# Performance work log

Hardware: AMD Instinct MI355X
Metric: run time of the kernel (lower is better)

## Reference

```python
import jax, jax.numpy as jnp
import numpy as np

EPS = 1e-05

def exp_map_at_origin(v, c):
    sqrt_c = jnp.sqrt(c)
    v_norm = jnp.maximum(jnp.linalg.norm(v, axis=-1, keepdims=True), EPS)
    return (1.0 / sqrt_c) * jnp.tanh(sqrt_c * v_norm) * (v / v_norm)

def log_map_at_origin(y, c):
    sqrt_c = jnp.sqrt(c)
    y_norm = jnp.maximum(jnp.linalg.norm(y, axis=-1, keepdims=True), EPS)
    y_norm_clamped = jnp.minimum(y_norm, 1.0 / sqrt_c - EPS)
    return (1.0 / sqrt_c) * jnp.arctanh(sqrt_c * y_norm_clamped) * (y / y_norm)

def poincare_distance(x, y, c):
    # x, y: [B, H, S, d]; returns [B, H, S, S]
    sqrt_c = jnp.sqrt(c)
    xns = jnp.sum(x * x, axis=-1, keepdims=True)          # [B,H,S,1]
    yns = jnp.sum(y * y, axis=-1, keepdims=True)          # [B,H,S,1]
    xy = jnp.einsum('bhsd,bhtd->bhst', x, y)
    xnsb = xns                                            # broadcast over t
    ynsb = jnp.swapaxes(yns, -2, -1)                      # [B,H,1,S]
    diff_norm_sq = xnsb - 2.0 * xy + ynsb
    denom = jnp.maximum((1.0 - c * xnsb) * (1.0 - c * ynsb), EPS)
    arg = jnp.maximum(1.0 + 2.0 * c * diff_norm_sq / denom, 1.0 + EPS)
    return (1.0 / sqrt_c) * jnp.arccosh(arg)

def setup_inputs() -> dict:
    key = jax.random.key(0)
    ks = jax.random.split(key, 5)
    B, S, D = 2, 1024, 1024
    x = jax.random.normal(ks[0], (B, S, D), dtype=jnp.float32)
    scale = 0.02
    W_q = scale * jax.random.normal(ks[1], (D, D), dtype=jnp.float32)
    W_k = scale * jax.random.normal(ks[2], (D, D), dtype=jnp.float32)
    W_v = scale * jax.random.normal(ks[3], (D, D), dtype=jnp.float32)
    W_o = scale * jax.random.normal(ks[4], (D, D), dtype=jnp.float32)
    return {
        'x': x, 'W_q': W_q, 'W_k': W_k, 'W_v': W_v, 'W_o': W_o,
        'log_c': jnp.zeros((), jnp.float32),
        'beta': jnp.zeros((), jnp.float32),
        'attention_bias': jnp.zeros((), jnp.float32),
    }

def reference(x, W_q, W_k, W_v, W_o, log_c, beta, attention_bias):
    B, S, D = x.shape
    H = 16
    dh = D // H
    c = jax.nn.softplus(log_c)
    beta_pos = jax.nn.softplus(beta)

    def split_heads(t):  # [B,S,D] -> [B,H,S,dh]
        return jnp.transpose(t.reshape(B, S, H, dh), (0, 2, 1, 3))

    q_t = split_heads(x @ W_q.T)
    k_t = split_heads(x @ W_k.T)
    v_t = split_heads(x @ W_v.T)

    q_h = exp_map_at_origin(q_t, c)
    k_h = exp_map_at_origin(k_t, c)
    v_h = exp_map_at_origin(v_t, c)

    dist = poincare_distance(q_h, k_h, c)                 # [B,H,S,S]
    scores = -beta_pos * dist - attention_bias
    weights = jax.nn.softmax(scores, axis=-1)

    v_tan = log_map_at_origin(v_h, c)
    out_tan = jnp.einsum('bhst,bhtd->bhsd', weights, v_tan)
    out_hyp = exp_map_at_origin(out_tan, c)
    out_heads_tan = log_map_at_origin(out_hyp, c)

    concat = jnp.transpose(out_heads_tan, (0, 2, 1, 3)).reshape(B, S, D)
    return concat @ W_o.T
```

## Files before the change

### kernel.cpp

```cpp
#include <hip/hip_runtime.h>
#include <math.h>


#define EPS_ 1e-5f

constexpr int Ss = 1024, Dd = 1024, Hh = 16, DHh = 64;

typedef __attribute__((ext_vector_type(8))) short bf16x8;
typedef __attribute__((ext_vector_type(4))) short s16x4;
typedef __attribute__((ext_vector_type(4))) float f32x4;

__device__ __forceinline__ float softplusf_(float x) {
    return (x > 20.f) ? x : log1pf(expf(x));
}
__device__ __forceinline__ short f2bf(float f) {
    union { float f; unsigned u; } v; v.f = f;
    unsigned r = v.u + 0x7FFFu + ((v.u >> 16) & 1u);
    return (short)(r >> 16);
}
__device__ __forceinline__ unsigned pks(short a, short b) {
    return (unsigned)(unsigned short)a | ((unsigned)(unsigned short)b << 16);
}

#if __has_builtin(__builtin_amdgcn_cvt_pk_bf16_f32)
typedef __attribute__((ext_vector_type(2))) __bf16 bfp2;
__device__ __forceinline__ unsigned cvtpk(float a, float b) {
    union { bfp2 v; unsigned u; } x;
    x.v = __builtin_amdgcn_cvt_pk_bf16_f32(a, b);
    return x.u;
}
#else
__device__ __forceinline__ unsigned cvtpk(float a, float b) { return pks(f2bf(a), f2bf(b)); }
#endif

#if __has_builtin(__builtin_amdgcn_sqrtf)
#define FSQRT __builtin_amdgcn_sqrtf
#else
#define FSQRT sqrtf
#endif
#if __has_builtin(__builtin_amdgcn_logf)
#define FLOG2 __builtin_amdgcn_logf
#else
#define FLOG2 __log2f
#endif
#if __has_builtin(__builtin_amdgcn_exp2f)
#define FEXP2 __builtin_amdgcn_exp2f
#else
#define FEXP2 exp2f
#endif

__device__ __forceinline__ void gload_lds16(const short* gp, short* lp) {
    __builtin_amdgcn_global_load_lds(
        (__attribute__((address_space(1))) void*)(void*)(const_cast<short*>(gp)),
        (__attribute__((address_space(3))) void*)(void*)(lp), 16, 0, 0);
}

__global__ __launch_bounds__(256) void split_all(
    const float* __restrict__ x,  const float* __restrict__ Wq,
    const float* __restrict__ Wk, const float* __restrict__ Wv,
    const float* __restrict__ Wo,
    short* __restrict__ xh,  short* __restrict__ wqh,
    short* __restrict__ wkh, short* __restrict__ wvh, short* __restrict__ woh)
{
    int g = blockIdx.x * 256 + threadIdx.x;
    const float* src; short* dst; int base;
    if (g < 524288)       { src = x;  dst = xh;  base = g; }
    else if (g < 786432)  { src = Wq; dst = wqh; base = g - 524288; }
    else if (g < 1048576) { src = Wk; dst = wkh; base = g - 786432; }
    else if (g < 1310720) { src = Wv; dst = wvh; base = g - 1048576; }
    else                  { src = Wo; dst = woh; base = g - 1310720; }
    float4 v = *(const float4*)(src + (size_t)base * 4);
    uint2 hp; hp.x = cvtpk(v.x, v.y); hp.y = cvtpk(v.z, v.w);
    *(uint2*)(dst + (size_t)base * 4) = hp;
}

__global__ __launch_bounds__(256, 3) void gemm_qkv(
    const short* __restrict__ Ap,
    const short* __restrict__ Wq, const short* __restrict__ Wk, const short* __restrict__ Wv,
    short* __restrict__ qh, short* __restrict__ kh, short* __restrict__ vtT,
    float* __restrict__ qnsT, float2* __restrict__ knpk,
    const float* __restrict__ p_logc)
{
    const int z = blockIdx.z;
    const short* Bp = (z == 0) ? Wq : (z == 1 ? Wk : Wv);
    const int K = 1024;

    __shared__ short As[128 * 64];
    __shared__ short Bs[64 * 64];

    const int tid = threadIdx.x;
    const int wv = tid >> 6, lane = tid & 63, quad = lane >> 4, l15 = lane & 15;
    const int bm = blockIdx.y * 128, bn = blockIdx.x * 64;

    const int lr8 = lane >> 3, lc8 = lane & 7;
    const int swz8 = (lc8 ^ lr8) * 8;

    const short* gAl = Ap + (size_t)(bm + lr8) * K + swz8;
    const short* gBl = Bp + (size_t)(bn + lr8) * K + swz8;

    f32x4 acc[2][4];
#pragma unroll
    for (int mt = 0; mt < 2; mt++)
#pragma unroll
        for (int j = 0; j < 4; j++) acc[mt][j] = (f32x4){0.f, 0.f, 0.f, 0.f};

    for (int k0 = 0; k0 < K; k0 += 64) {
        __syncthreads();
#pragma unroll
        for (int i = 0; i < 4; i++)
            gload_lds16(gAl + (size_t)((wv * 4 + i) * 8) * K + k0, &As[(wv * 4 + i) * 512]);
#pragma unroll
        for (int j = 0; j < 2; j++)
            gload_lds16(gBl + (size_t)((wv * 2 + j) * 8) * K + k0, &Bs[(wv * 2 + j) * 512]);
        __syncthreads();
#pragma unroll
        for (int w = 0; w < 2; w++) {
            const int xs = ((w * 4 + quad) ^ (l15 & 7)) * 8;
            bf16x8 fa0 = *(const bf16x8*)&As[(wv * 32 + l15) * 64 + xs];
            bf16x8 fa1 = *(const bf16x8*)&As[(wv * 32 + 16 + l15) * 64 + xs];
#pragma unroll
            for (int nt = 0; nt < 4; nt++) {
                bf16x8 fb = *(const bf16x8*)&Bs[(nt * 16 + l15) * 64 + xs];
                acc[0][nt] = __builtin_amdgcn_mfma_f32_16x16x32_bf16(fa0, fb, acc[0][nt], 0, 0, 0);
                acc[1][nt] = __builtin_amdgcn_mfma_f32_16x16x32_bf16(fa1, fb, acc[1][nt], 0, 0, 0);
            }
        }
    }

    const float c = softplusf_(p_logc[0]);
    const float sc = sqrtf(c);
    const float twoC = 2.f * c;
    const int h0 = blockIdx.x;

    if (z < 2) {
        short* yout = (z == 0) ? qh : kh;
#pragma unroll
        for (int mt = 0; mt < 2; mt++) {
            const int mbase = bm + wv * 32 + mt * 16;
            float fr[4];
#pragma unroll
            for (int r = 0; r < 4; r++) {
                float s2 = 0.f;
#pragma unroll
                for (int nt = 0; nt < 4; nt++) s2 += acc[mt][nt][r] * acc[mt][nt][r];
#pragma unroll
                for (int mk = 1; mk < 16; mk <<= 1) s2 += __shfl_xor(s2, mk, 64);
                float n = fmaxf(sqrtf(s2), EPS_);
                float fac = tanhf(sc * n) / (sc * n);
                fr[r] = fac;
                if (l15 == 0) {
                    int m = mbase + quad * 4 + r;
                    int bI = m >> 10, s = m & 1023;
                    float yns = s2 * fac * fac;
                    if (z == 0) {
                        qnsT[(size_t)(bI * Hh + h0) * Ss + s] = yns;
                    } else {
                        knpk[(size_t)(bI * Hh + h0) * Ss + s]
                            = make_float2(yns, twoC / (1.f - c * yns));
                    }
                }
            }
#pragma unroll
            for (int nt = 0; nt < 4; nt++)
#pragma unroll
                for (int r = 0; r < 4; r++) {
                    int m = mbase + quad * 4 + r;
                    yout[(size_t)m * Dd + bn + nt * 16 + l15] = f2bf(acc[mt][nt][r] * fr[r]);
                }
        }
    } else {
#pragma unroll
        for (int mt = 0; mt < 2; mt++) {
            const int mbase = bm + wv * 32 + mt * 16;
            float tr[4];
#pragma unroll
            for (int r = 0; r < 4; r++) {
                float s2 = 0.f;
#pragma unroll
                for (int nt = 0; nt < 4; nt++) s2 += acc[mt][nt][r] * acc[mt][nt][r];
#pragma unroll
                for (int mk = 1; mk < 16; mk <<= 1) s2 += __shfl_xor(s2, mk, 64);
                float n = fmaxf(sqrtf(s2), EPS_);
                float fac = tanhf(sc * n) / (sc * n);
                float yn = n * fac;
                float ycl = fminf(yn, 1.f / sc - EPS_);
                float f2 = atanhf(sc * ycl) / (sc * fmaxf(yn, EPS_));
                tr[r] = fac * f2;
            }
            const int m0 = mbase + quad * 4;
            const int bI = m0 >> 10, s0 = m0 & 1023;
            const int w6 = s0 & 63;
            const int s0p = (s0 & ~63)
                          | ((w6 >> 5) * 32 + ((w6 & 15) >> 2) * 8 + ((w6 >> 4) & 1) * 4);
#pragma unroll
            for (int nt = 0; nt < 4; nt++) {
                int d = nt * 16 + l15;
                uint2 pk;
                pk.x = cvtpk(acc[mt][nt][0] * tr[0], acc[mt][nt][1] * tr[1]);
                pk.y = cvtpk(acc[mt][nt][2] * tr[2], acc[mt][nt][3] * tr[3]);
                *(uint2*)&vtT[((size_t)(bI * Hh + h0) * DHh + d) * Ss + s0p] = pk;
            }
        }
    }
}

__global__ __launch_bounds__(512) void attn_mfma(
    const short* __restrict__ qh, const short* __restrict__ kh, const short* __restrict__ vtT,
    const float* __restrict__ qnsT, const float2* __restrict__ knpk,
    short* __restrict__ ccb,
    const float* __restrict__ p_logc, const float* __restrict__ p_beta)
{
    const float c = softplusf_(p_logc[0]);
    const float sc = sqrtf(c);
    const float bp = softplusf_(p_beta[0]);
    const float nkc = -bp / sc;
    const float cap = 2.f * c * 1e5f;
    const float onePlus = 1.f + EPS_;

    const int bh = blockIdx.x, qt = blockIdx.y;
    const int b = bh >> 4, h = bh & 15;
    const int tid = threadIdx.x;
    const int wv = tid >> 6, lane = tid & 63;
    const int g = wv >> 2, w4 = wv & 3;
    const int quad = lane >> 4, l15 = lane & 15;
    const int q = qt * 64 + w4 * 16 + l15;

    __shared__ short Ks[2][2][4096];
    __shared__ short Vt[2][2][4096];

    const short* qb = qh + (size_t)(b * Ss + q) * Dd + h * DHh + quad * 8;
    bf16x8 qf0 = *(const bf16x8*)qb;
    bf16x8 qf1 = *(const bf16x8*)(qb + 32);

    const float qn = qnsT[(size_t)bh * Ss + q];
    const float irq = 1.f / (1.f - c * qn);

    f32x4 O4[4];
#pragma unroll
    for (int nt = 0; nt < 4; nt++) O4[nt] = (f32x4){0.f, 0.f, 0.f, 0.f};
    float lac = 0.f;

    const int tbase = g * 512;
    const int lr8 = lane >> 3, lc8 = lane & 7;
    const float2* nb = knpk + (size_t)bh * Ss;
    const short* ksb = kh + (size_t)b * Ss * Dd + h * DHh + (lc8 ^ lr8) * 8;
    const short* vsb = vtT + (size_t)bh * DHh * Ss + tbase + (lc8 ^ lr8) * 8;

    f32x4 nA0[4], nA1[4], nB0[4], nB1[4];

#pragma unroll
    for (int j = 0; j < 2; j++) {
        const int R = w4 * 16 + j * 8;
        gload_lds16(ksb + (size_t)(tbase + R + lr8) * Dd, &Ks[g][0][R * 64]);
        gload_lds16(vsb + (size_t)(R + lr8) * Ss, &Vt[g][0][R * 64]);
        gload_lds16(ksb + (size_t)(tbase + 64 + R + lr8) * Dd, &Ks[g][1][R * 64]);
        gload_lds16(vsb + (size_t)(R + lr8) * Ss + 64, &Vt[g][1][R * 64]);
    }
#pragma unroll
    for (int nt = 0; nt < 4; nt++) {
        const float2* np = nb + tbase + nt * 16 + quad * 4;
        nA0[nt] = *(const f32x4*)np;
        nA1[nt] = *(const f32x4*)(np + 2);
    }
    __syncthreads();

    const int xsl = (quad ^ (l15 & 7)) * 8;

#pragma unroll
    for (int ch = 0; ch < 8; ch++) {
        const int cur = ch & 1;

        bf16x8 k0[4], k1[4], v0[4], v1[4];
#pragma unroll
        for (int nt = 0; nt < 4; nt++) {
            k0[nt] = *(const bf16x8*)&Ks[g][cur][(nt * 16 + l15) * 64 + xsl];
            k1[nt] = *(const bf16x8*)&Ks[g][cur][(nt * 16 + l15) * 64 + (xsl ^ 32)];
        }
#pragma unroll
        for (int nt = 0; nt < 4; nt++) {
            v0[nt] = *(const bf16x8*)&Vt[g][cur][(nt * 16 + l15) * 64 + xsl];
            v1[nt] = *(const bf16x8*)&Vt[g][cur][(nt * 16 + l15) * 64 + (xsl ^ 32)];
        }

        f32x4 acc[4];
        __builtin_amdgcn_s_setprio(1);
#pragma unroll
        for (int nt = 0; nt < 4; nt++) {
            f32x4 a = (f32x4){0.f, 0.f, 0.f, 0.f};
            a = __builtin_amdgcn_mfma_f32_16x16x32_bf16(k0[nt], qf0, a, 0, 0, 0);
            a = __builtin_amdgcn_mfma_f32_16x16x32_bf16(k1[nt], qf1, a, 0, 0, 0);
            acc[nt] = a;
        }
        __builtin_amdgcn_s_setprio(0);

        if (ch < 7) __syncthreads();

        if (ch + 2 < 8) {
#pragma unroll
            for (int j = 0; j < 2; j++) {
                const int R = w4 * 16 + j * 8;
                gload_lds16(ksb + (size_t)(tbase + (ch + 2) * 64 + R + lr8) * Dd,
                            &Ks[g][cur][R * 64]);
                gload_lds16(vsb + (size_t)(R + lr8) * Ss + (ch + 2) * 64,
                            &Vt[g][cur][R * 64]);
            }
        }
        if (ch + 1 < 8) {
#pragma unroll
            for (int nt = 0; nt < 4; nt++) {
                const float2* np = nb + tbase + (ch + 1) * 64 + nt * 16 + quad * 4;
                if ((ch & 1) == 0) { nB0[nt] = *(const f32x4*)np; nB1[nt] = *(const f32x4*)(np + 2); }
                else               { nA0[nt] = *(const f32x4*)np; nA1[nt] = *(const f32x4*)(np + 2); }
            }
        }

        float sv[4][4];
#pragma unroll
        for (int nt = 0; nt < 4; nt++) {
#pragma unroll
            for (int r = 0; r < 4; r++) {
                float kn, ik2c;
                if ((ch & 1) == 0) {
                    kn   = (r < 2) ? nA0[nt][(r & 1) * 2]     : nA1[nt][(r & 1) * 2];
                    ik2c = (r < 2) ? nA0[nt][(r & 1) * 2 + 1] : nA1[nt][(r & 1) * 2 + 1];
                } else {
                    kn   = (r < 2) ? nB0[nt][(r & 1) * 2]     : nB1[nt][(r & 1) * 2];
                    ik2c = (r < 2) ? nB0[nt][(r & 1) * 2 + 1] : nB1[nt][(r & 1) * 2 + 1];
                }
                float dns = (qn + kn) - 2.f * acc[nt][r];
                float co  = fminf(irq * ik2c, cap);
                float arg = fmaxf(fmaf(co, dns, 1.f), onePlus);
                float u   = arg + FSQRT(fmaf(arg, arg, -1.f));
                float p   = FEXP2(nkc * FLOG2(u));
                sv[nt][r] = p;
                lac += p;
            }
        }

        union { unsigned u[4]; bf16x8 v; } p0, p1;
        p0.u[0] = cvtpk(sv[0][0], sv[0][1]); p0.u[1] = cvtpk(sv[0][2], sv[0][3]);
        p0.u[2] = cvtpk(sv[1][0], sv[1][1]); p0.u[3] = cvtpk(sv[1][2], sv[1][3]);
        p1.u[0] = cvtpk(sv[2][0], sv[2][1]); p1.u[1] = cvtpk(sv[2][2], sv[2][3]);
        p1.u[2] = cvtpk(sv[3][0], sv[3][1]); p1.u[3] = cvtpk(sv[3][2], sv[3][3]);

        __builtin_amdgcn_s_setprio(1);
#pragma unroll
        for (int nt = 0; nt < 4; nt++) {
            O4[nt] = __builtin_amdgcn_mfma_f32_16x16x32_bf16(v0[nt], p0.v, O4[nt], 0, 0, 0);
            O4[nt] = __builtin_amdgcn_mfma_f32_16x16x32_bf16(v1[nt], p1.v, O4[nt], 0, 0, 0);
        }
        __builtin_amdgcn_s_setprio(0);
    }

    lac += __shfl_xor(lac, 16, 64);
    lac += __shfl_xor(lac, 32, 64);

    float* Ored = (float*)&Ks[0][0][0];
    float* lred = (float*)&Vt[0][0][0];
    __syncthreads();
    if (g == 1) {
#pragma unroll
        for (int nt = 0; nt < 4; nt++)
#pragma unroll
            for (int r = 0; r < 4; r++)
                Ored[((w4 * 4 + nt) * 16 + (quad * 4 + r)) * 16 + l15] = O4[nt][r];
        if (lane < 16) lred[w4 * 16 + lane] = lac;
    }
    __syncthreads();

    if (g == 0) {
        const float lt = lac + lred[w4 * 16 + l15];
        const float il = 1.f / lt;
        float ot[4][4], t2 = 0.f;
#pragma unroll
        for (int nt = 0; nt < 4; nt++)
#pragma unroll
            for (int r = 0; r < 4; r++) {
                float v = (O4[nt][r]
                    + Ored[((w4 * 4 + nt) * 16 + (quad * 4 + r)) * 16 + l15]) * il;
                ot[nt][r] = v;
                t2 += v * v;
            }
        t2 += __shfl_xor(t2, 16, 64);
        t2 += __shfl_xor(t2, 32, 64);

        float n = fmaxf(sqrtf(t2), EPS_);
        float fac = tanhf(sc * n) / (sc * n);
        float y2 = t2 * fac * fac;
        float yn = fmaxf(sqrtf(y2), EPS_);
        float ycl = fminf(yn, 1.f / sc - EPS_);
        float fac2 = atanhf(sc * ycl) / (sc * yn);
        float tot = fac * fac2;

        short* ob = ccb + (size_t)(b * Ss + q) * Dd + h * DHh;
#pragma unroll
        for (int nt = 0; nt < 4; nt++) {
            uint2 pk;
            pk.x = cvtpk(ot[nt][0] * tot, ot[nt][1] * tot);
            pk.y = cvtpk(ot[nt][2] * tot, ot[nt][3] * tot);
            *(uint2*)(ob + nt * 16 + quad * 4) = pk;
        }
    }
}

__global__ __launch_bounds__(256, 6) void gemm_out(
    const short* __restrict__ Ap, const short* __restrict__ Bp,
    float* __restrict__ Cp)
{
    const int K = 1024, N = 1024;
    __shared__ short As[64 * 64];
    __shared__ short Bs[64 * 64];
    const int tid = threadIdx.x;
    const int wv = tid >> 6, lane = tid & 63, quad = lane >> 4, l15 = lane & 15;
    const int bm = blockIdx.y * 64, bn = blockIdx.x * 64;

    const int lr8 = lane >> 3, lc8 = lane & 7;
    const int swz8 = (lc8 ^ lr8) * 8;

    const short* gAl = Ap + (size_t)(bm + lr8) * K + swz8;
    const short* gBl = Bp + (size_t)(bn + lr8) * K + swz8;

    f32x4 acc[4];
#pragma unroll
    for (int j = 0; j < 4; j++) acc[j] = (f32x4){0.f, 0.f, 0.f, 0.f};

    for (int k0 = 0; k0 < K; k0 += 64) {
        __syncthreads();
#pragma unroll
        for (int j = 0; j < 2; j++) {
            gload_lds16(gAl + (size_t)((wv * 2 + j) * 8) * K + k0, &As[(wv * 2 + j) * 512]);
            gload_lds16(gBl + (size_t)((wv * 2 + j) * 8) * K + k0, &Bs[(wv * 2 + j) * 512]);
        }
        __syncthreads();
#pragma unroll
        for (int w = 0; w < 2; w++) {
            const int xs = ((w * 4 + quad) ^ (l15 & 7)) * 8;
            bf16x8 fa = *(const bf16x8*)&As[(wv * 16 + l15) * 64 + xs];
#pragma unroll
            for (int nt = 0; nt < 4; nt++) {
                bf16x8 fb = *(const bf16x8*)&Bs[(nt * 16 + l15) * 64 + xs];
                acc[nt] = __builtin_amdgcn_mfma_f32_16x16x32_bf16(fa, fb, acc[nt], 0, 0, 0);
            }
        }
    }
#pragma unroll
    for (int nt = 0; nt < 4; nt++)
#pragma unroll
        for (int r = 0; r < 4; r++)
            Cp[(size_t)(bm + wv * 16 + quad * 4 + r) * N + bn + nt * 16 + l15] = acc[nt][r];
}

extern "C" void kernel_launch(void* const* d_in, const int* in_sizes, int n_in,
                              void* d_out, int out_size, void* d_ws, size_t ws_size,
                              hipStream_t stream)
{
    const float* x    = (const float*)d_in[0];
    const float* Wq   = (const float*)d_in[1];
    const float* Wk   = (const float*)d_in[2];
    const float* Wv   = (const float*)d_in[3];
    const float* Wo   = (const float*)d_in[4];
    const float* logc = (const float*)d_in[5];
    const float* beta = (const float*)d_in[6];
    float* out = (float*)d_out;

    const size_t M2 = 2097152, M1 = 1048576;
    short* ws    = (short*)d_ws;
    short* xh    = ws;
    short* wqh   = xh + M2;
    short* wkh   = wqh + M1;
    short* wvh   = wkh + M1;
    short* woh   = wvh + M1;
    short* qh    = woh + M1;
    short* kh    = qh + M2;
    short* vtT   = kh + M2;
    float* qnsT  = (float*)(vtT + M2);
    float2* knpk = (float2*)(qnsT + 32768);
    short* ccb   = xh;

    split_all<<<dim3(6144), 256, 0, stream>>>(x, Wq, Wk, Wv, Wo, xh, wqh, wkh, wvh, woh);
    gemm_qkv<<<dim3(16, 16, 3), 256, 0, stream>>>(xh, wqh, wkh, wvh,
        qh, kh, vtT, qnsT, knpk, logc);
    attn_mfma<<<dim3(32, 16, 1), 512, 0, stream>>>(qh, kh, vtT, qnsT, knpk,
        ccb, logc, beta);
    gemm_out<<<dim3(16, 32), 256, 0, stream>>>(ccb, woh, out);
}
```

Before: 156.0 us.

## Drop key-split across wave groups in attention; one group walks all keys

The attention kernel used two groups of four waves, each covering half the key range, then merged partial outputs and row sums through shared memory. Now a 256-thread block has four waves that each walk all 16 key chunks, which removes the cross-group reduction, its extra barriers and half the shared memory. The grid stays at 512 blocks, so the waves in flight halve while each wave does twice as many serial iterations. The lower LDS and register use may raise blocks per CU to make up for that.

```diff
diff --git a/kernel.cpp b/kernel.cpp
--- a/kernel.cpp
+++ b/kernel.cpp
@@ -204,7 +204,7 @@
     }
 }
 
-__global__ __launch_bounds__(512) void attn_mfma(
+__global__ __launch_bounds__(256, 4) void attn_mfma(
     const short* __restrict__ qh, const short* __restrict__ kh, const short* __restrict__ vtT,
     const float* __restrict__ qnsT, const float2* __restrict__ knpk,
     short* __restrict__ ccb,
@@ -221,12 +221,11 @@
     const int b = bh >> 4, h = bh & 15;
     const int tid = threadIdx.x;
     const int wv = tid >> 6, lane = tid & 63;
-    const int g = wv >> 2, w4 = wv & 3;
     const int quad = lane >> 4, l15 = lane & 15;
-    const int q = qt * 64 + w4 * 16 + l15;
-
-    __shared__ short Ks[2][2][4096];
-    __shared__ short Vt[2][2][4096];
+    const int q = qt * 64 + wv * 16 + l15;
+
+    __shared__ short Ks[2][4096];
+    __shared__ short Vt[2][4096];
 
     const short* qb = qh + (size_t)(b * Ss + q) * Dd + h * DHh + quad * 8;
     bf16x8 qf0 = *(const bf16x8*)qb;
@@ -240,25 +239,24 @@
     for (int nt = 0; nt < 4; nt++) O4[nt] = (f32x4){0.f, 0.f, 0.f, 0.f};
     float lac = 0.f;
 
-    const int tbase = g * 512;
     const int lr8 = lane >> 3, lc8 = lane & 7;
     const float2* nb = knpk + (size_t)bh * Ss;
     const short* ksb = kh + (size_t)b * Ss * Dd + h * DHh + (lc8 ^ lr8) * 8;
-    const short* vsb = vtT + (size_t)bh * DHh * Ss + tbase + (lc8 ^ lr8) * 8;
+    const short* vsb = vtT + (size_t)bh * DHh * Ss + (lc8 ^ lr8) * 8;
 
     f32x4 nA0[4], nA1[4], nB0[4], nB1[4];
 
 #pragma unroll
     for (int j = 0; j < 2; j++) {
-        const int R = w4 * 16 + j * 8;
-        gload_lds16(ksb + (size_t)(tbase + R + lr8) * Dd, &Ks[g][0][R * 64]);
-        gload_lds16(vsb + (size_t)(R + lr8) * Ss, &Vt[g][0][R * 64]);
-        gload_lds16(ksb + (size_t)(tbase + 64 + R + lr8) * Dd, &Ks[g][1][R * 64]);
-        gload_lds16(vsb + (size_t)(R + lr8) * Ss + 64, &Vt[g][1][R * 64]);
+        const int R = wv * 16 + j * 8;
+        gload_lds16(ksb + (size_t)(R + lr8) * Dd, &Ks[0][R * 64]);
+        gload_lds16(vsb + (size_t)(R + lr8) * Ss, &Vt[0][R * 64]);
+        gload_lds16(ksb + (size_t)(64 + R + lr8) * Dd, &Ks[1][R * 64]);
+        gload_lds16(vsb + (size_t)(R + lr8) * Ss + 64, &Vt[1][R * 64]);
     }
 #pragma unroll
     for (int nt = 0; nt < 4; nt++) {
-        const float2* np = nb + tbase + nt * 16 + quad * 4;
+        const float2* np = nb + nt * 16 + quad * 4;
         nA0[nt] = *(const f32x4*)np;
         nA1[nt] = *(const f32x4*)(np + 2);
     }
@@ -267,19 +265,19 @@
     const int xsl = (quad ^ (l15 & 7)) * 8;
 
 #pragma unroll
-    for (int ch = 0; ch < 8; ch++) {
+    for (int ch = 0; ch < 16; ch++) {
         const int cur = ch & 1;
 
         bf16x8 k0[4], k1[4], v0[4], v1[4];
 #pragma unroll
         for (int nt = 0; nt < 4; nt++) {
-            k0[nt] = *(const bf16x8*)&Ks[g][cur][(nt * 16 + l15) * 64 + xsl];
-            k1[nt] = *(const bf16x8*)&Ks[g][cur][(nt * 16 + l15) * 64 + (xsl ^ 32)];
+            k0[nt] = *(const bf16x8*)&Ks[cur][(nt * 16 + l15) * 64 + xsl];
+            k1[nt] = *(const bf16x8*)&Ks[cur][(nt * 16 + l15) * 64 + (xsl ^ 32)];
         }
 #pragma unroll
         for (int nt = 0; nt < 4; nt++) {
-            v0[nt] = *(const bf16x8*)&Vt[g][cur][(nt * 16 + l15) * 64 + xsl];
-            v1[nt] = *(const bf16x8*)&Vt[g][cur][(nt * 16 + l15) * 64 + (xsl ^ 32)];
+            v0[nt] = *(const bf16x8*)&Vt[cur][(nt * 16 + l15) * 64 + xsl];
+            v1[nt] = *(const bf16x8*)&Vt[cur][(nt * 16 + l15) * 64 + (xsl ^ 32)];
         }
 
         f32x4 acc[4];
@@ -293,22 +291,22 @@
         }
         __builtin_amdgcn_s_setprio(0);
 
-        if (ch < 7) __syncthreads();
-
-        if (ch + 2 < 8) {
+        if (ch < 15) __syncthreads();
+
+        if (ch + 2 < 16) {
 #pragma unroll
             for (int j = 0; j < 2; j++) {
-                const int R = w4 * 16 + j * 8;
-                gload_lds16(ksb + (size_t)(tbase + (ch + 2) * 64 + R + lr8) * Dd,
-                            &Ks[g][cur][R * 64]);
+                const int R = wv * 16 + j * 8;
+                gload_lds16(ksb + (size_t)((ch + 2) * 64 + R + lr8) * Dd,
+                            &Ks[cur][R * 64]);
                 gload_lds16(vsb + (size_t)(R + lr8) * Ss + (ch + 2) * 64,
-                            &Vt[g][cur][R * 64]);
-            }
-        }
-        if (ch + 1 < 8) {
+                            &Vt[cur][R * 64]);
+            }
+        }
+        if (ch + 1 < 16) {
 #pragma unroll
             for (int nt = 0; nt < 4; nt++) {
-                const float2* np = nb + tbase + (ch + 1) * 64 + nt * 16 + quad * 4;
+                const float2* np = nb + (ch + 1) * 64 + nt * 16 + quad * 4;
                 if ((ch & 1) == 0) { nB0[nt] = *(const f32x4*)np; nB1[nt] = *(const f32x4*)(np + 2); }
                 else               { nA0[nt] = *(const f32x4*)np; nA1[nt] = *(const f32x4*)(np + 2); }
             }
@@ -354,52 +352,35 @@
 
     lac += __shfl_xor(lac, 16, 64);
     lac += __shfl_xor(lac, 32, 64);
-
-    float* Ored = (float*)&Ks[0][0][0];
-    float* lred = (float*)&Vt[0][0][0];
-    __syncthreads();
-    if (g == 1) {
-#pragma unroll
-        for (int nt = 0; nt < 4; nt++)
-#pragma unroll
-            for (int r = 0; r < 4; r++)
-                Ored[((w4 * 4 + nt) * 16 + (quad * 4 + r)) * 16 + l15] = O4[nt][r];
-        if (lane < 16) lred[w4 * 16 + lane] = lac;
-    }
-    __syncthreads();
-
-    if (g == 0) {
-        const float lt = lac + lred[w4 * 16 + l15];
-        const float il = 1.f / lt;
-        float ot[4][4], t2 = 0.f;
-#pragma unroll
-        for (int nt = 0; nt < 4; nt++)
-#pragma unroll
-            for (int r = 0; r < 4; r++) {
-                float v = (O4[nt][r]
-                    + Ored[((w4 * 4 + nt) * 16 + (quad * 4 + r)) * 16 + l15]) * il;
-                ot[nt][r] = v;
-                t2 += v * v;
-            }
-        t2 += __shfl_xor(t2, 16, 64);
-        t2 += __shfl_xor(t2, 32, 64);
-
-        float n = fmaxf(sqrtf(t2), EPS_);
-        float fac = tanhf(sc * n) / (sc * n);
-        float y2 = t2 * fac * fac;
-        float yn = fmaxf(sqrtf(y2), EPS_);
-        float ycl = fminf(yn, 1.f / sc - EPS_);
-        float fac2 = atanhf(sc * ycl) / (sc * yn);
-        float tot = fac * fac2;
-
-        short* ob = ccb + (size_t)(b * Ss + q) * Dd + h * DHh;
-#pragma unroll
-        for (int nt = 0; nt < 4; nt++) {
-            uint2 pk;
-            pk.x = cvtpk(ot[nt][0] * tot, ot[nt][1] * tot);
-            pk.y = cvtpk(ot[nt][2] * tot, ot[nt][3] * tot);
-            *(uint2*)(ob + nt * 16 + quad * 4) = pk;
-        }
+    const float il = 1.f / lac;
+
+    float ot[4][4], t2 = 0.f;
+#pragma unroll
+    for (int nt = 0; nt < 4; nt++)
+#pragma unroll
+        for (int r = 0; r < 4; r++) {
+            float v = O4[nt][r] * il;
+            ot[nt][r] = v;
+            t2 += v * v;
+        }
+    t2 += __shfl_xor(t2, 16, 64);
+    t2 += __shfl_xor(t2, 32, 64);
+
+    float n = fmaxf(sqrtf(t2), EPS_);
+    float fac = tanhf(sc * n) / (sc * n);
+    float y2 = t2 * fac * fac;
+    float yn = fmaxf(sqrtf(y2), EPS_);
+    float ycl = fminf(yn, 1.f / sc - EPS_);
+    float fac2 = atanhf(sc * ycl) / (sc * yn);
+    float tot = fac * fac2;
+
+    short* ob = ccb + (size_t)(b * Ss + q) * Dd + h * DHh;
+#pragma unroll
+    for (int nt = 0; nt < 4; nt++) {
+        uint2 pk;
+        pk.x = cvtpk(ot[nt][0] * tot, ot[nt][1] * tot);
+        pk.y = cvtpk(ot[nt][2] * tot, ot[nt][3] * tot);
+        *(uint2*)(ob + nt * 16 + quad * 4) = pk;
     }
 }
 
@@ -480,7 +461,7 @@
     split_all<<<dim3(6144), 256, 0, stream>>>(x, Wq, Wk, Wv, Wo, xh, wqh, wkh, wvh, woh);
     gemm_qkv<<<dim3(16, 16, 3), 256, 0, stream>>>(xh, wqh, wkh, wvh,
         qh, kh, vtT, qnsT, knpk, logc);
-    attn_mfma<<<dim3(32, 16, 1), 512, 0, stream>>>(qh, kh, vtT, qnsT, knpk,
+    attn_mfma<<<dim3(32, 16, 1), 256, 0, stream>>>(qh, kh, vtT, qnsT, knpk,
         ccb, logc, beta);
     gemm_out<<<dim3(16, 32), 256, 0, stream>>>(ccb, woh, out);
 }
```

Result: slower. 210.5 us (+35.0%).
